# Kernel optimization log

Hardware: AMD Instinct MI355X
Metric: run time of the kernel (lower is better)

The kernel has to match this reference:

```python
import jax, jax.numpy as jnp
import numpy as np

B, N, IN_DIM, OUT_DIM = 8, 2048, 128, 128
NEG_SLOPE = 0.2

def setup_inputs() -> dict:
    key = jax.random.key(0)
    k1, k2, k3, k4 = jax.random.split(key, 4)
    x = jax.random.normal(k1, (B, N, IN_DIM), dtype=jnp.float32)
    adj = jax.random.randint(k2, (N, N), 0, 2, dtype=jnp.int32)
    # nn.Linear weight init scale ~ 1/sqrt(fan_in)
    W = jax.random.normal(k3, (IN_DIM, OUT_DIM), dtype=jnp.float32) / np.sqrt(IN_DIM)
    a_vec = jax.random.normal(k4, (2 * OUT_DIM,), dtype=jnp.float32) / np.sqrt(2 * OUT_DIM)
    return {"x": x, "adj": adj, "W": W, "a_vec": a_vec}

def reference(x, adj, W, a_vec):
    # h = x @ W : [b, n, d]
    h = jnp.einsum("bni,io->bno", x, W)
    # Algebraic decomposition of a([h_i, h_j]) = a1.h_i + a2.h_j
    a1, a2 = a_vec[:OUT_DIM], a_vec[OUT_DIM:]
    s_i = h @ a1  # [b, n] score contribution from source node i
    s_j = h @ a2  # [b, n] score contribution from target node j
    e = s_i[:, :, None] + s_j[:, None, :]  # [b, n, n]
    e = jnp.where(e >= 0, e, NEG_SLOPE * e)  # leaky_relu(0.2)
    mask = (adj > 0)[None, :, :]  # [1, n, n] broadcast over batch
    e = jnp.where(mask, e, -jnp.inf)
    alpha = jax.nn.softmax(e, axis=-1)  # [b, n, n]
    out = jnp.einsum("bnm,bmd->bnd", alpha, h)  # [b, n, d]
    return out, alpha
```

## Files before the change

kernel.cpp:

```cpp
#include <hip/hip_runtime.h>
#include <hip/hip_bf16.h>
#include <cstdint>
#include <cstddef>

constexpr int Bn = 8;
constexpr int Nn = 2048;
constexpr int Dn = 128;

typedef __bf16 bf16x8 __attribute__((ext_vector_type(8)));
typedef float f32x4 __attribute__((ext_vector_type(4)));

#define AS1 __attribute__((address_space(1)))
#define AS3 __attribute__((address_space(3)))

static __device__ __forceinline__ void gl_lds16(const void* g, void* l) {
  __builtin_amdgcn_global_load_lds((AS1 const void*)g, (AS3 void*)l, 16, 0, 0);
}

__global__ __launch_bounds__(256) void gat_k1(
    const float* __restrict__ x, const float* __restrict__ W,
    const float* __restrict__ a_vec,
    __bf16* __restrict__ hT, float* __restrict__ s1, float* __restrict__ s2) {
  __shared__ __align__(16) float Wl[64 * 144];
  __shared__ __align__(16) float xL[32 * 132];

  const int t = threadIdx.x;
  const int r0 = blockIdx.x * 32;
  const int b = r0 >> 11;
  const int n0 = r0 & (Nn - 1);
  const int rp = (t >> 4) << 1;
  const int c0 = (t & 15) << 3;
  const int c0p = c0 + ((c0 >> 5) << 2);

  float acc[2][8];
#pragma unroll
  for (int r = 0; r < 2; ++r)
#pragma unroll
    for (int c = 0; c < 8; ++c) acc[r][c] = 0.f;

#pragma unroll
  for (int it = 0; it < 4; ++it) {
    int idx = t + (it << 8);
    int rr = idx >> 5, kc = (idx & 31) << 2;
    *(float4*)(xL + rr * 132 + kc) = *(const float4*)(x + (size_t)(r0 + rr) * Dn + kc);
  }

  for (int ph = 0; ph < 2; ++ph) {
    if (ph) __syncthreads();
#pragma unroll
    for (int it = 0; it < 8; ++it) {
      int idx = t + (it << 8);
      int kk = idx >> 5, c4 = (idx & 31) << 2;
      int dsto = kk * 144 + c4 + ((c4 >> 5) << 2);
      *(float4*)(Wl + dsto) = *(const float4*)(W + (size_t)((ph << 6) + kk) * Dn + c4);
    }
    __syncthreads();
    const float* xrow = xL + rp * 132 + (ph << 6);
    for (int k = 0; k < 64; ++k) {
      float xa0 = xrow[k];
      float xa1 = xrow[132 + k];
      float4 w0 = *(const float4*)(Wl + k * 144 + c0p);
      float4 w1 = *(const float4*)(Wl + k * 144 + c0p + 4);
      float ws[8] = {w0.x, w0.y, w0.z, w0.w, w1.x, w1.y, w1.z, w1.w};
#pragma unroll
      for (int c = 0; c < 8; ++c) {
        acc[0][c] = fmaf(xa0, ws[c], acc[0][c]);
        acc[1][c] = fmaf(xa1, ws[c], acc[1][c]);
      }
    }
  }

  float q1[2] = {0.f, 0.f}, q2[2] = {0.f, 0.f};
#pragma unroll
  for (int c = 0; c < 8; ++c) {
    float a1c = a_vec[c0 + c];
    float a2c = a_vec[Dn + c0 + c];
    q1[0] = fmaf(acc[0][c], a1c, q1[0]);
    q1[1] = fmaf(acc[1][c], a1c, q1[1]);
    q2[0] = fmaf(acc[0][c], a2c, q2[0]);
    q2[1] = fmaf(acc[1][c], a2c, q2[1]);
  }
#pragma unroll
  for (int d = 1; d < 16; d <<= 1) {
    q1[0] += __shfl_xor(q1[0], d);
    q1[1] += __shfl_xor(q1[1], d);
    q2[0] += __shfl_xor(q2[0], d);
    q2[1] += __shfl_xor(q2[1], d);
  }
  if ((t & 15) == 0) {
    s1[b * Nn + n0 + rp] = q1[0];
    s1[b * Nn + n0 + rp + 1] = q1[1];
    s2[b * Nn + n0 + rp] = q2[0];
    s2[b * Nn + n0 + rp + 1] = q2[1];
  }

#pragma unroll
  for (int c = 0; c < 8; ++c) {
    union { __bf16 h[2]; uint32_t u; } pk;
    pk.h[0] = (__bf16)acc[0][c];
    pk.h[1] = (__bf16)acc[1][c];
    *(uint32_t*)(hT + (size_t)(b * Dn + c0 + c) * Nn + n0 + rp) = pk.u;
  }
}

__global__ __launch_bounds__(512) void gat_k2(
    const int* __restrict__ adj, const __bf16* __restrict__ hT,
    const float* __restrict__ s1, const float* __restrict__ s2,
    float* __restrict__ out, float* __restrict__ alpha) {
  __shared__ __align__(16) float sj[Nn];
  __shared__ float siv[32], invl[32];
  __shared__ __align__(16) __bf16 Pl[2][32 * 72];
  __shared__ __align__(16) __bf16 hl[2][128 * 64];

  const int t = threadIdx.x;
  const int b = blockIdx.x >> 6;
  const int i0 = (blockIdx.x & 63) << 5;
  const int w = t >> 6, lane = t & 63;
  const int ii = t >> 4, sub = t & 15;
  const int lrow = lane >> 3, ccs = lane & 7;
  const __bf16* __restrict__ hTb = hT + (size_t)b * Dn * Nn;

#pragma unroll
  for (int inst = 0; inst < 2; ++inst) {
    int row = (w << 4) + (inst << 3) + lrow;
    gl_lds16(hTb + (size_t)row * Nn + ((ccs ^ lrow) << 3),
             &hl[0][((w << 4) + (inst << 3)) << 6]);
  }

  *(float4*)(sj + (t << 2)) = *(const float4*)(s2 + b * Nn + (t << 2));
  if (t < 32) siv[t] = s1[b * Nn + i0 + t];
  __syncthreads();

  const int i = i0 + ii;
  const int* __restrict__ adjrow = adj + (size_t)i * Nn;
  const float si = siv[ii];

  float l = 0.f;
  for (int cc = 0; cc < 32; ++cc) {
    int j = (cc << 6) + (sub << 2);
    int4 am = *(const int4*)(adjrow + j);
    float4 sv = *(const float4*)(sj + j);
    float e;
    e = si + sv.x; e = fmaxf(e, 0.2f * e); l += (am.x > 0) ? __expf(e) : 0.f;
    e = si + sv.y; e = fmaxf(e, 0.2f * e); l += (am.y > 0) ? __expf(e) : 0.f;
    e = si + sv.z; e = fmaxf(e, 0.2f * e); l += (am.z > 0) ? __expf(e) : 0.f;
    e = si + sv.w; e = fmaxf(e, 0.2f * e); l += (am.w > 0) ? __expf(e) : 0.f;
  }
  l += __shfl_xor(l, 1);
  l += __shfl_xor(l, 2);
  l += __shfl_xor(l, 4);
  l += __shfl_xor(l, 8);
  if (sub == 0) invl[ii] = 1.f / l;
  __syncthreads();
  const float il = invl[ii];

  const int iw = (w & 1) << 4;
  const int nd0 = (w >> 1) << 5;
  const int q16 = lane >> 4, m16 = lane & 15;
  f32x4 acc0 = {0.f, 0.f, 0.f, 0.f}, acc1 = {0.f, 0.f, 0.f, 0.f};
  float* __restrict__ arow = alpha + ((size_t)(b * Nn + i) << 11);

  for (int jt = 0; jt < 32; ++jt) {
    const int buf = jt & 1;
    const int j0 = jt << 6;
    {
      int j = j0 + (sub << 2);
      int4 am = *(const int4*)(adjrow + j);
      float4 sv = *(const float4*)(sj + j);
      float e0 = si + sv.x; e0 = fmaxf(e0, 0.2f * e0);
      float e1 = si + sv.y; e1 = fmaxf(e1, 0.2f * e1);
      float e2 = si + sv.z; e2 = fmaxf(e2, 0.2f * e2);
      float e3 = si + sv.w; e3 = fmaxf(e3, 0.2f * e3);
      float a0 = (am.x > 0) ? __expf(e0) * il : 0.f;
      float a1 = (am.y > 0) ? __expf(e1) * il : 0.f;
      float a2 = (am.z > 0) ? __expf(e2) * il : 0.f;
      float a3 = (am.w > 0) ? __expf(e3) * il : 0.f;
      *(float4*)(arow + j) = make_float4(a0, a1, a2, a3);
      union { __bf16 h[4]; uint2 u; } pk;
      pk.h[0] = (__bf16)a0; pk.h[1] = (__bf16)a1;
      pk.h[2] = (__bf16)a2; pk.h[3] = (__bf16)a3;
      *(uint2*)(&Pl[buf][ii * 72 + (sub << 2)]) = pk.u;
    }
    __syncthreads();
    if (jt < 31) {
      int jn = j0 + 64;
#pragma unroll
      for (int inst = 0; inst < 2; ++inst) {
        int row = (w << 4) + (inst << 3) + lrow;
        gl_lds16(hTb + (size_t)row * Nn + jn + ((ccs ^ lrow) << 3),
                 &hl[buf ^ 1][((w << 4) + (inst << 3)) << 6]);
      }
    }
#pragma unroll
    for (int ks = 0; ks < 2; ++ks) {
      bf16x8 af = *(const bf16x8*)(&Pl[buf][(iw + m16) * 72 + (ks << 5) + (q16 << 3)]);
      {
        int d = nd0 + m16;
        int phys = ((ks << 2) + q16) ^ (d & 7);
        bf16x8 bv = *(const bf16x8*)(&hl[buf][(d << 6) + (phys << 3)]);
        acc0 = __builtin_amdgcn_mfma_f32_16x16x32_bf16(af, bv, acc0, 0, 0, 0);
      }
      {
        int d = nd0 + 16 + m16;
        int phys = ((ks << 2) + q16) ^ (d & 7);
        bf16x8 bv = *(const bf16x8*)(&hl[buf][(d << 6) + (phys << 3)]);
        acc1 = __builtin_amdgcn_mfma_f32_16x16x32_bf16(af, bv, acc1, 0, 0, 0);
      }
    }
  }

#pragma unroll
  for (int nb = 0; nb < 2; ++nb) {
    f32x4 a = nb ? acc1 : acc0;
    int d = nd0 + (nb << 4) + m16;
#pragma unroll
    for (int r = 0; r < 4; ++r) {
      int irow = i0 + iw + (q16 << 2) + r;
      out[((size_t)(b * Nn + irow) << 7) + d] = a[r];
    }
  }
}

extern "C" void kernel_launch(void* const* d_in, const int* in_sizes, int n_in,
                              void* d_out, int out_size, void* d_ws, size_t ws_size,
                              hipStream_t stream) {
  const float* x = (const float*)d_in[0];
  const int* adj = (const int*)d_in[1];
  const float* W = (const float*)d_in[2];
  const float* a_vec = (const float*)d_in[3];

  float* out = (float*)d_out;
  float* alpha = out + (size_t)Bn * Nn * Dn;

  char* ws = (char*)d_ws;
  __bf16* hT = (__bf16*)ws;
  float* s1 = (float*)(ws + (size_t)Bn * Dn * Nn * 2);
  float* s2 = s1 + (size_t)Bn * Nn;

  gat_k1<<<512, 256, 0, stream>>>(x, W, a_vec, hT, s1, s2);
  gat_k2<<<512, 512, 0, stream>>>(adj, hT, s1, s2, out, alpha);
}
```

Baseline: 194.1 us.

## Pack adjacency into bitmask and interleave batch across blocks

Adds a pre-pass kernel that ballots the int32 adjacency matrix into a 64-bit-per-64-entries bitmask. The main kernel then reads mask words instead of int4 adjacency vectors, which cuts adjacency traffic that was previously read twice per batch. The block-to-(batch,row) mapping is also changed so that consecutive blocks share the same adjacency rows across batches, which should improve cache reuse. The cost is one extra launch that reads the full 16 MB adjacency once, plus bit extraction work inside the kernel.

```diff
diff --git a/kernel.cpp b/kernel.cpp
--- a/kernel.cpp
+++ b/kernel.cpp
@@ -15,6 +15,15 @@
 
 static __device__ __forceinline__ void gl_lds16(const void* g, void* l) {
   __builtin_amdgcn_global_load_lds((AS1 const void*)g, (AS3 void*)l, 16, 0, 0);
+}
+
+__global__ __launch_bounds__(256) void gat_k0(
+    const int* __restrict__ adj, unsigned long long* __restrict__ mask64) {
+  const int t = threadIdx.x;
+  const size_t g = (size_t)blockIdx.x * 256 + t;
+  int v = adj[g];
+  unsigned long long bal = __ballot(v > 0);
+  if ((t & 63) == 0) mask64[g >> 6] = bal;
 }
 
 __global__ __launch_bounds__(256) void gat_k1(
@@ -104,7 +113,7 @@
 }
 
 __global__ __launch_bounds__(512) void gat_k2(
-    const int* __restrict__ adj, const __bf16* __restrict__ hT,
+    const uint32_t* __restrict__ mask, const __bf16* __restrict__ hT,
     const float* __restrict__ s1, const float* __restrict__ s2,
     float* __restrict__ out, float* __restrict__ alpha) {
   __shared__ __align__(16) float sj[Nn];
@@ -113,8 +122,8 @@
   __shared__ __align__(16) __bf16 hl[2][128 * 64];
 
   const int t = threadIdx.x;
-  const int b = blockIdx.x >> 6;
-  const int i0 = (blockIdx.x & 63) << 5;
+  const int b = blockIdx.x & 7;
+  const int i0 = (blockIdx.x >> 3) << 5;
   const int w = t >> 6, lane = t & 63;
   const int ii = t >> 4, sub = t & 15;
   const int lrow = lane >> 3, ccs = lane & 7;
@@ -132,19 +141,21 @@
   __syncthreads();
 
   const int i = i0 + ii;
-  const int* __restrict__ adjrow = adj + (size_t)i * Nn;
+  const uint32_t* __restrict__ mrow = mask + ((size_t)i << 6);
   const float si = siv[ii];
 
   float l = 0.f;
+  const int wofs = sub >> 3;
+  const int bsh = (sub & 7) << 2;
   for (int cc = 0; cc < 32; ++cc) {
     int j = (cc << 6) + (sub << 2);
-    int4 am = *(const int4*)(adjrow + j);
+    uint32_t mw = mrow[(cc << 1) + wofs];
     float4 sv = *(const float4*)(sj + j);
     float e;
-    e = si + sv.x; e = fmaxf(e, 0.2f * e); l += (am.x > 0) ? __expf(e) : 0.f;
-    e = si + sv.y; e = fmaxf(e, 0.2f * e); l += (am.y > 0) ? __expf(e) : 0.f;
-    e = si + sv.z; e = fmaxf(e, 0.2f * e); l += (am.z > 0) ? __expf(e) : 0.f;
-    e = si + sv.w; e = fmaxf(e, 0.2f * e); l += (am.w > 0) ? __expf(e) : 0.f;
+    e = si + sv.x; e = fmaxf(e, 0.2f * e); l += ((mw >> (bsh + 0)) & 1u) ? __expf(e) : 0.f;
+    e = si + sv.y; e = fmaxf(e, 0.2f * e); l += ((mw >> (bsh + 1)) & 1u) ? __expf(e) : 0.f;
+    e = si + sv.z; e = fmaxf(e, 0.2f * e); l += ((mw >> (bsh + 2)) & 1u) ? __expf(e) : 0.f;
+    e = si + sv.w; e = fmaxf(e, 0.2f * e); l += ((mw >> (bsh + 3)) & 1u) ? __expf(e) : 0.f;
   }
   l += __shfl_xor(l, 1);
   l += __shfl_xor(l, 2);
@@ -165,16 +176,16 @@
     const int j0 = jt << 6;
     {
       int j = j0 + (sub << 2);
-      int4 am = *(const int4*)(adjrow + j);
+      uint32_t mw = mrow[(j0 >> 5) + wofs];
       float4 sv = *(const float4*)(sj + j);
       float e0 = si + sv.x; e0 = fmaxf(e0, 0.2f * e0);
       float e1 = si + sv.y; e1 = fmaxf(e1, 0.2f * e1);
       float e2 = si + sv.z; e2 = fmaxf(e2, 0.2f * e2);
       float e3 = si + sv.w; e3 = fmaxf(e3, 0.2f * e3);
-      float a0 = (am.x > 0) ? __expf(e0) * il : 0.f;
-      float a1 = (am.y > 0) ? __expf(e1) * il : 0.f;
-      float a2 = (am.z > 0) ? __expf(e2) * il : 0.f;
-      float a3 = (am.w > 0) ? __expf(e3) * il : 0.f;
+      float a0 = ((mw >> (bsh + 0)) & 1u) ? __expf(e0) * il : 0.f;
+      float a1 = ((mw >> (bsh + 1)) & 1u) ? __expf(e1) * il : 0.f;
+      float a2 = ((mw >> (bsh + 2)) & 1u) ? __expf(e2) * il : 0.f;
+      float a3 = ((mw >> (bsh + 3)) & 1u) ? __expf(e3) * il : 0.f;
       *(float4*)(arow + j) = make_float4(a0, a1, a2, a3);
       union { __bf16 h[4]; uint2 u; } pk;
       pk.h[0] = (__bf16)a0; pk.h[1] = (__bf16)a1;
@@ -236,7 +247,9 @@
   __bf16* hT = (__bf16*)ws;
   float* s1 = (float*)(ws + (size_t)Bn * Dn * Nn * 2);
   float* s2 = s1 + (size_t)Bn * Nn;
-
+  unsigned long long* mask64 = (unsigned long long*)(s2 + (size_t)Bn * Nn);
+
+  gat_k0<<<(Nn * Nn) / 256, 256, 0, stream>>>(adj, mask64);
   gat_k1<<<512, 256, 0, stream>>>(x, W, a_vec, hT, s1, s2);
-  gat_k2<<<512, 512, 0, stream>>>(adj, hT, s1, s2, out, alpha);
-}
+  gat_k2<<<512, 512, 0, stream>>>((const uint32_t*)mask64, hT, s1, s2, out, alpha);
+}
```

Result: slower. 200.9 us (+3.5%).
